# Performance work log

Measured on AMD Instinct MI355X. Metric: run time of the kernel, lower is better.

Reference implementation:

```python
import jax, jax.numpy as jnp
import numpy as np

D_MODEL = 768
N_HEADS = 12
D_K = D_MODEL // N_HEADS


def setup_inputs() -> dict:
    key = jax.random.key(0)
    ks = jax.random.split(key, 9)
    s = 1.0 / np.sqrt(D_MODEL)
    return {
        "x": jax.random.normal(ks[0], (2, 2048, D_MODEL), dtype=jnp.float32),
        "w_q": jax.random.normal(ks[1], (D_MODEL, D_MODEL), dtype=jnp.float32) * s,
        "b_q": jax.random.normal(ks[2], (D_MODEL,), dtype=jnp.float32) * 0.02,
        "w_k": jax.random.normal(ks[3], (D_MODEL, D_MODEL), dtype=jnp.float32) * s,
        "b_k": jax.random.normal(ks[4], (D_MODEL,), dtype=jnp.float32) * 0.02,
        "w_v": jax.random.normal(ks[5], (D_MODEL, D_MODEL), dtype=jnp.float32) * s,
        "b_v": jax.random.normal(ks[6], (D_MODEL,), dtype=jnp.float32) * 0.02,
        "w_o": jax.random.normal(ks[7], (D_MODEL, D_MODEL), dtype=jnp.float32) * s,
        "b_o": jax.random.normal(ks[8], (D_MODEL,), dtype=jnp.float32) * 0.02,
    }


def reference(x, w_q, b_q, w_k, b_k, w_v, b_v, w_o, b_o):
    B, S, _ = x.shape
    # nn.Linear: y = x @ W^T + b
    def proj(w, b):
        y = jnp.einsum("bsd,ed->bse", x, w) + b
        # [B, S, D] -> [B, H, S, d_k]
        return y.reshape(B, S, N_HEADS, D_K).transpose(0, 2, 1, 3)

    q = proj(w_q, b_q)
    k = proj(w_k, b_k)
    v = proj(w_v, b_v)

    scale = 1.0 / np.sqrt(D_K).astype(np.float32)
    scores = jnp.einsum("bhqd,bhkd->bhqk", q, k) * scale  # [B,H,S,S]
    attn = jax.nn.softmax(scores, axis=-1)
    ctx = jnp.einsum("bhqk,bhkd->bhqd", attn, v)  # [B,H,S,d_k]
    ctx = ctx.transpose(0, 2, 1, 3).reshape(B, S, D_MODEL)
    out = jnp.einsum("bsd,ed->bse", ctx, w_o) + b_o
    return out
```

## Files before the change

### kernel.cpp

```cpp
#include <hip/hip_runtime.h>
#include <hip/hip_bf16.h>

#define B_   2
#define S_   2048
#define D_   768
#define H_   12
#define DK_  64
#define R_   (B_*S_)
#define LOG2E_OVER8 0.18033688011112042f

typedef __attribute__((ext_vector_type(8))) short short8;
typedef __attribute__((ext_vector_type(4))) float f32x4;

__device__ __forceinline__ short f2b(float f) {
  union { float f; unsigned u; } x; x.f = f;
  unsigned r = x.u + 0x7fffu + ((x.u >> 16) & 1u);
  return (short)(r >> 16);
}

__device__ __forceinline__ unsigned cvt_pk_bf16(float lo, float hi) {
  unsigned r;
  asm("v_cvt_pk_bf16_f32 %0, %1, %2" : "=v"(r) : "v"(lo), "v"(hi));
  return r;
}

__device__ __forceinline__ void gl_lds16(const short* g, short* l) {
  __builtin_amdgcn_global_load_lds(
      (const __attribute__((address_space(1))) void*)g,
      (__attribute__((address_space(3))) void*)l, 16, 0, 0);
}

__global__ void cvt_kernel(const float* __restrict__ x,
                           const float* __restrict__ wq, const float* __restrict__ wk,
                           const float* __restrict__ wv, const float* __restrict__ wo,
                           short* __restrict__ xb, short* __restrict__ wb) {
  const int XQ = R_ * D_ / 4;
  const int WQ = D_ * D_ / 4;
  int idx = blockIdx.x * blockDim.x + threadIdx.x;
  const float* src; short* dst; int off;
  if (idx < XQ) { src = x; dst = xb; off = idx; }
  else {
    int wi = idx - XQ; int w = wi / WQ; off = wi - w * WQ;
    if      (w == 0) { src = wq; dst = wb; }
    else if (w == 1) { src = wk; dst = wb + D_*D_; }
    else if (w == 2) { src = wv; dst = wb + 2*D_*D_; }
    else             { src = wo; dst = wb + 3*D_*D_; }
  }
  float4 v = ((const float4*)src)[off];
  short4 o;
  o.x = f2b(v.x); o.y = f2b(v.y); o.z = f2b(v.z); o.w = f2b(v.w);
  ((short4*)dst)[off] = o;
}

__launch_bounds__(256)
__global__ void qkv_gemm_kernel(const short* __restrict__ xb, const short* __restrict__ wb,
                                const float* __restrict__ bq, const float* __restrict__ bk,
                                const float* __restrict__ bv,
                                short* __restrict__ Qw, short* __restrict__ Kw,
                                short* __restrict__ VTw) {
  __shared__ short As[2][128 * 32];
  __shared__ short Bs[2][128 * 32];
  const int which = blockIdx.z;
  const short* W = wb + which * (D_ * D_);
  const float* bias = (which == 0) ? bq : (which == 1) ? bk : bv;
  const int n0 = blockIdx.x * 128, m0 = blockIdx.y * 128;
  const int t = threadIdx.x, l = t & 63, w = t >> 6;
  const int wr = w >> 1, wc = w & 1;

  f32x4 acc[4][4] = {};
  const int srow = t >> 2, sseg = (t & 3) * 8;

#define GSTAGE(buf, k0) do { \
    gl_lds16(xb + (m0 + srow) * D_ + (k0) + sseg,      &As[buf][t * 8]); \
    gl_lds16(xb + (m0 + 64 + srow) * D_ + (k0) + sseg, &As[buf][(t + 256) * 8]); \
    gl_lds16(W  + (n0 + srow) * D_ + (k0) + sseg,      &Bs[buf][t * 8]); \
    gl_lds16(W  + (n0 + 64 + srow) * D_ + (k0) + sseg, &Bs[buf][(t + 256) * 8]); \
  } while (0)

  GSTAGE(0, 0);
  __syncthreads();
  int cur = 0;
  for (int k0 = 0; k0 < D_; k0 += 32) {
    if (k0 + 32 < D_) GSTAGE(cur ^ 1, k0 + 32);
    short8 a[4], b[4];
#pragma unroll
    for (int i = 0; i < 4; i++)
      a[i] = *(const short8*)&As[cur][(wr * 64 + i * 16 + (l & 15)) * 32 + (l >> 4) * 8];
#pragma unroll
    for (int i = 0; i < 4; i++)
      b[i] = *(const short8*)&Bs[cur][(wc * 64 + i * 16 + (l & 15)) * 32 + (l >> 4) * 8];
#pragma unroll
    for (int i = 0; i < 4; i++)
#pragma unroll
      for (int j = 0; j < 4; j++)
        acc[i][j] = __builtin_amdgcn_mfma_f32_16x16x32_bf16(a[i], b[j], acc[i][j], 0, 0, 0);
    __syncthreads();
    cur ^= 1;
  }
#undef GSTAGE

#pragma unroll
  for (int i = 0; i < 4; i++) {
#pragma unroll
    for (int j2 = 0; j2 < 4; j2++) {
      int mm = m0 + wr * 64 + i * 16 + (l >> 4) * 4 + j2;
      int bidx = mm >> 11, s = mm & 2047;
#pragma unroll
      for (int nj = 0; nj < 4; nj++) {
        int e = n0 + wc * 64 + nj * 16 + (l & 15);
        float val = acc[i][nj][j2] + bias[e];
        int h = e >> 6, dk = e & 63;
        int bh = bidx * H_ + h;
        if (which == 0)      Qw[(bh * S_ + s) * DK_ + dk] = f2b(val * LOG2E_OVER8);
        else if (which == 1) Kw[(bh * S_ + s) * DK_ + dk] = f2b(val);
        else                 VTw[(bh * DK_ + dk) * S_ + s] = f2b(val);
      }
    }
  }
}

#define KVB   32
#define SHALF 1024
__launch_bounds__(256, 3)
__global__ void attn_kernel(const short* __restrict__ Qw, const short* __restrict__ Kw,
                            const short* __restrict__ VTw, short* __restrict__ ctx) {
  __shared__ short Ksh[2][2][KVB * DK_];
  __shared__ short Vsh[2][2][KVB * DK_];

  const int t = threadIdx.x, l = t & 63, w = t >> 6;
  const int s = w >> 1, qh = w & 1;
  const int L = blockIdx.y * 32 + blockIdx.x;
  const int xcd = L & 7, idx = L >> 3;
  const int bh = xcd * 3 + (idx >> 5);
  const int qblk = idx & 31;
  const int q0 = qblk * 64 + qh * 32;
  const int bq = bh / H_, h = bh - bq * H_;
  const short* Qh = Qw + bh * S_ * DK_;
  const short* Kh = Kw + (bh * S_ + s * SHALF) * DK_;
  const short* Vh = VTw + bh * DK_ * S_ + s * SHALF;

  const int tt = t & 127;
  const int kr0 = tt >> 3, kc0 = tt & 7;
  const int koff0 = kr0 * DK_ + ((kc0 ^ (kr0 & 7)) << 3);
  const int vc8 = (tt & 7) ^ ((tt >> 3) & 7);
  const int vr0 = 2 * (tt >> 3) + (vc8 >> 2);
  const int voff0 = vr0 * S_ + ((vc8 & 3) << 3);

#define STAGE(buf, kt) do { \
    gl_lds16(Kh + (kt) * DK_ + koff0,        &Ksh[s][buf][tt * 8]); \
    gl_lds16(Kh + (kt) * DK_ + koff0 + 1024, &Ksh[s][buf][tt * 8 + 1024]); \
    gl_lds16(Vh + (kt) + voff0,              &Vsh[s][buf][tt * 8]); \
    gl_lds16(Vh + (kt) + voff0 + 32 * S_,    &Vsh[s][buf][tt * 8 + 1024]); \
  } while (0)

  short8 qf[2][2];
#pragma unroll
  for (int mi = 0; mi < 2; mi++)
#pragma unroll
    for (int ks = 0; ks < 2; ks++)
      qf[mi][ks] = *(const short8*)&Qh[(q0 + 16 * mi + (l & 15)) * DK_ + ks * 32 + (l >> 4) * 8];

  f32x4 acc_o[2][4] = {};
  float l_run[2] = {0.f, 0.f};

  STAGE(0, 0);
  __syncthreads();
  int cur = 0;

  for (int kt = 0; kt < SHALF; kt += KVB) {
    if (kt + KVB < SHALF) STAGE(cur ^ 1, kt + KVB);

    f32x4 acc_s[2][2] = {};
    __builtin_amdgcn_s_setprio(1);
#pragma unroll
    for (int ni = 0; ni < 2; ni++) {
      int r = (l & 15) + 16 * ni;
#pragma unroll
      for (int ks = 0; ks < 2; ks++) {
        int cc = (l >> 4) + 4 * ks;
        short8 kf = *(const short8*)&Ksh[s][cur][r * DK_ + ((cc ^ (r & 7)) << 3)];
        acc_s[0][ni] = __builtin_amdgcn_mfma_f32_16x16x32_bf16(kf, qf[0][ks], acc_s[0][ni], 0, 0, 0);
        acc_s[1][ni] = __builtin_amdgcn_mfma_f32_16x16x32_bf16(kf, qf[1][ks], acc_s[1][ni], 0, 0, 0);
      }
    }
    __builtin_amdgcn_s_setprio(0);

#pragma unroll
    for (int mi = 0; mi < 2; mi++) {
      float sum = 0.f;
#pragma unroll
      for (int ni = 0; ni < 2; ni++)
#pragma unroll
        for (int j = 0; j < 4; j++) {
          float p = __builtin_amdgcn_exp2f(acc_s[mi][ni][j]);
          acc_s[mi][ni][j] = p;
          sum += p;
        }
      l_run[mi] += sum;
    }

    union PK { unsigned u[4]; short8 v; } pa0, pa1;
    pa0.u[0] = cvt_pk_bf16(acc_s[0][0][0], acc_s[0][0][1]);
    pa0.u[1] = cvt_pk_bf16(acc_s[0][0][2], acc_s[0][0][3]);
    pa0.u[2] = cvt_pk_bf16(acc_s[0][1][0], acc_s[0][1][1]);
    pa0.u[3] = cvt_pk_bf16(acc_s[0][1][2], acc_s[0][1][3]);
    pa1.u[0] = cvt_pk_bf16(acc_s[1][0][0], acc_s[1][0][1]);
    pa1.u[1] = cvt_pk_bf16(acc_s[1][0][2], acc_s[1][0][3]);
    pa1.u[2] = cvt_pk_bf16(acc_s[1][1][0], acc_s[1][1][1]);
    pa1.u[3] = cvt_pk_bf16(acc_s[1][1][2], acc_s[1][1][3]);

    __builtin_amdgcn_s_setprio(1);
    {
      const int cc = l >> 4;
      union V8 { short4 h[2]; short8 v; };
#pragma unroll
      for (int nd = 0; nd < 4; nd++) {
        int vr = (l & 15) + 16 * nd, rp = vr >> 1;
        int ph0 = (((vr & 1) << 2) | (cc >> 1)) ^ (rp & 7);
        int ph1 = (((vr & 1) << 2) | (2 + (cc >> 1))) ^ (rp & 7);
        V8 vf;
        vf.h[0] = *(const short4*)&Vsh[s][cur][rp * 64 + ph0 * 8 + (cc & 1) * 4];
        vf.h[1] = *(const short4*)&Vsh[s][cur][rp * 64 + ph1 * 8 + (cc & 1) * 4];
        acc_o[0][nd] = __builtin_amdgcn_mfma_f32_16x16x32_bf16(pa0.v, vf.v, acc_o[0][nd], 0, 0, 0);
        acc_o[1][nd] = __builtin_amdgcn_mfma_f32_16x16x32_bf16(pa1.v, vf.v, acc_o[1][nd], 0, 0, 0);
      }
    }
    __builtin_amdgcn_s_setprio(0);

    __syncthreads();
    cur ^= 1;
  }

#pragma unroll
  for (int mi = 0; mi < 2; mi++) {
    l_run[mi] += __shfl_xor(l_run[mi], 16);
    l_run[mi] += __shfl_xor(l_run[mi], 32);
  }

  __syncthreads();
  float* Oshf = (float*)&Ksh[0][0][0];
  float* Lsh  = (float*)&Vsh[0][0][0];
  if (s == 1) {
#pragma unroll
    for (int mi = 0; mi < 2; mi++)
#pragma unroll
      for (int nd = 0; nd < 4; nd++)
#pragma unroll
        for (int j = 0; j < 4; j++)
          Oshf[qh * 2048 + (16 * mi + (l >> 4) * 4 + j) * 64 + (l & 15) + 16 * nd] = acc_o[mi][nd][j];
    if (l < 16) {
      Lsh[(qh * 2 + 0) * 16 + l] = l_run[0];
      Lsh[(qh * 2 + 1) * 16 + l] = l_run[1];
    }
  }
  __syncthreads();
  if (s == 0) {
#pragma unroll
    for (int mi = 0; mi < 2; mi++) {
#pragma unroll
      for (int j = 0; j < 4; j++) {
        int src = ((l >> 4) << 2) + j;
        float llo = __shfl(l_run[mi], src);
        float lhi = Lsh[(qh * 2 + mi) * 16 + src];
        float inv = 1.f / (llo + lhi);
        int srow = q0 + 16 * mi + src;
#pragma unroll
        for (int nd = 0; nd < 4; nd++) {
          float ohi = Oshf[qh * 2048 + (16 * mi + src) * 64 + (l & 15) + 16 * nd];
          float val = (acc_o[mi][nd][j] + ohi) * inv;
          ctx[(bq * S_ + srow) * D_ + h * DK_ + (l & 15) + 16 * nd] = f2b(val);
        }
      }
    }
  }
#undef STAGE
}

__launch_bounds__(256)
__global__ void oproj_kernel(const short* __restrict__ ctx, const short* __restrict__ Wo,
                             const float* __restrict__ bo, float* __restrict__ out) {
  __shared__ short As[2][128 * 32];
  __shared__ short Bs[2][128 * 32];
  const int n0 = blockIdx.x * 128, m0 = blockIdx.y * 128;
  const int t = threadIdx.x, l = t & 63, w = t >> 6;
  const int wr = w >> 1, wc = w & 1;

  f32x4 acc[4][4] = {};
  const int srow = t >> 2, sseg = (t & 3) * 8;

#define GSTAGE(buf, k0) do { \
    gl_lds16(ctx + (m0 + srow) * D_ + (k0) + sseg,      &As[buf][t * 8]); \
    gl_lds16(ctx + (m0 + 64 + srow) * D_ + (k0) + sseg, &As[buf][(t + 256) * 8]); \
    gl_lds16(Wo  + (n0 + srow) * D_ + (k0) + sseg,      &Bs[buf][t * 8]); \
    gl_lds16(Wo  + (n0 + 64 + srow) * D_ + (k0) + sseg, &Bs[buf][(t + 256) * 8]); \
  } while (0)

  GSTAGE(0, 0);
  __syncthreads();
  int cur = 0;
  for (int k0 = 0; k0 < D_; k0 += 32) {
    if (k0 + 32 < D_) GSTAGE(cur ^ 1, k0 + 32);
    short8 a[4], b[4];
#pragma unroll
    for (int i = 0; i < 4; i++)
      a[i] = *(const short8*)&As[cur][(wr * 64 + i * 16 + (l & 15)) * 32 + (l >> 4) * 8];
#pragma unroll
    for (int i = 0; i < 4; i++)
      b[i] = *(const short8*)&Bs[cur][(wc * 64 + i * 16 + (l & 15)) * 32 + (l >> 4) * 8];
#pragma unroll
    for (int i = 0; i < 4; i++)
#pragma unroll
      for (int j = 0; j < 4; j++)
        acc[i][j] = __builtin_amdgcn_mfma_f32_16x16x32_bf16(a[i], b[j], acc[i][j], 0, 0, 0);
    __syncthreads();
    cur ^= 1;
  }
#undef GSTAGE

#pragma unroll
  for (int i = 0; i < 4; i++) {
#pragma unroll
    for (int j2 = 0; j2 < 4; j2++) {
      int mm = m0 + wr * 64 + i * 16 + (l >> 4) * 4 + j2;
#pragma unroll
      for (int nj = 0; nj < 4; nj++) {
        int e = n0 + wc * 64 + nj * 16 + (l & 15);
        out[mm * D_ + e] = acc[i][nj][j2] + bo[e];
      }
    }
  }
}

extern "C" void kernel_launch(void* const* d_in, const int* in_sizes, int n_in,
                              void* d_out, int out_size, void* d_ws, size_t ws_size,
                              hipStream_t stream) {
  (void)in_sizes; (void)n_in; (void)out_size; (void)ws_size;
  const float* x  = (const float*)d_in[0];
  const float* wq = (const float*)d_in[1];
  const float* bq = (const float*)d_in[2];
  const float* wk = (const float*)d_in[3];
  const float* bk = (const float*)d_in[4];
  const float* wv = (const float*)d_in[5];
  const float* bv = (const float*)d_in[6];
  const float* wo = (const float*)d_in[7];
  const float* bo = (const float*)d_in[8];
  float* out = (float*)d_out;

  short* xb  = (short*)d_ws;
  short* wb  = xb + R_ * D_;
  short* Qw  = wb + 4 * D_ * D_;
  short* Kw  = Qw + R_ * D_;
  short* VTw = Kw + R_ * D_;
  short* ctx = VTw + R_ * D_;

  cvt_kernel<<<5376, 256, 0, stream>>>(x, wq, wk, wv, wo, xb, wb);
  qkv_gemm_kernel<<<dim3(6, 32, 3), 256, 0, stream>>>(xb, wb, bq, bk, bv, Qw, Kw, VTw);
  attn_kernel<<<dim3(32, 24), 256, 0, stream>>>(Qw, Kw, VTw, ctx);
  oproj_kernel<<<dim3(6, 32), 256, 0, stream>>>(ctx, wb + 3 * D_ * D_, bo, out);
}
```

Measured before the change: 97.40 us.

## Split attention KV range four ways per block, each wave covering all 64 queries

Restructures the attention kernel so each of the four waves takes a quarter of the key/value sequence (512 keys) and processes all 64 query rows, instead of two KV halves times two 32-row query halves. Each K/V fragment loaded from LDS now feeds four MFMAs instead of two, which cuts LDS read traffic per unit of compute. The cost is more accumulator registers per wave, occupancy lowered from 3 to 2 blocks, and a larger four-way partial sum reduction through shared memory at the end.

```diff
diff --git a/kernel.cpp b/kernel.cpp
--- a/kernel.cpp
+++ b/kernel.cpp
@@ -119,58 +119,58 @@
   }
 }
 
-#define KVB   32
-#define SHALF 1024
-__launch_bounds__(256, 3)
+#define KVB  32
+#define SQTR 512
+__launch_bounds__(256, 2)
 __global__ void attn_kernel(const short* __restrict__ Qw, const short* __restrict__ Kw,
                             const short* __restrict__ VTw, short* __restrict__ ctx) {
-  __shared__ short Ksh[2][2][KVB * DK_];
-  __shared__ short Vsh[2][2][KVB * DK_];
-
-  const int t = threadIdx.x, l = t & 63, w = t >> 6;
-  const int s = w >> 1, qh = w & 1;
+  __shared__ short Ksh[4][2][KVB * DK_];
+  __shared__ short Vsh[4][2][KVB * DK_];
+  __shared__ float Lsh[3][64];
+
+  const int t = threadIdx.x, l = t & 63, s = t >> 6;
   const int L = blockIdx.y * 32 + blockIdx.x;
   const int xcd = L & 7, idx = L >> 3;
   const int bh = xcd * 3 + (idx >> 5);
   const int qblk = idx & 31;
-  const int q0 = qblk * 64 + qh * 32;
+  const int q0 = qblk * 64;
   const int bq = bh / H_, h = bh - bq * H_;
   const short* Qh = Qw + bh * S_ * DK_;
-  const short* Kh = Kw + (bh * S_ + s * SHALF) * DK_;
-  const short* Vh = VTw + bh * DK_ * S_ + s * SHALF;
-
-  const int tt = t & 127;
-  const int kr0 = tt >> 3, kc0 = tt & 7;
-  const int koff0 = kr0 * DK_ + ((kc0 ^ (kr0 & 7)) << 3);
-  const int vc8 = (tt & 7) ^ ((tt >> 3) & 7);
-  const int vr0 = 2 * (tt >> 3) + (vc8 >> 2);
+  const short* Kh = Kw + (bh * S_ + s * SQTR) * DK_;
+  const short* Vh = VTw + bh * DK_ * S_ + s * SQTR;
+
+  const int c0 = l & 7, r0 = l >> 3;
+  const int koff0 = r0 * DK_ + ((c0 ^ r0) << 3);
+  const int vc8 = c0 ^ r0;
+  const int vr0 = 2 * r0 + (vc8 >> 2);
   const int voff0 = vr0 * S_ + ((vc8 & 3) << 3);
 
 #define STAGE(buf, kt) do { \
-    gl_lds16(Kh + (kt) * DK_ + koff0,        &Ksh[s][buf][tt * 8]); \
-    gl_lds16(Kh + (kt) * DK_ + koff0 + 1024, &Ksh[s][buf][tt * 8 + 1024]); \
-    gl_lds16(Vh + (kt) + voff0,              &Vsh[s][buf][tt * 8]); \
-    gl_lds16(Vh + (kt) + voff0 + 32 * S_,    &Vsh[s][buf][tt * 8 + 1024]); \
+    _Pragma("unroll") \
+    for (int j = 0; j < 4; j++) { \
+      gl_lds16(Kh + (kt) * DK_ + koff0 + 512 * j, &Ksh[s][buf][l * 8 + 512 * j]); \
+      gl_lds16(Vh + (kt) + voff0 + 16 * S_ * j,   &Vsh[s][buf][l * 8 + 512 * j]); \
+    } \
   } while (0)
 
-  short8 qf[2][2];
-#pragma unroll
-  for (int mi = 0; mi < 2; mi++)
+  short8 qf[4][2];
+#pragma unroll
+  for (int mi = 0; mi < 4; mi++)
 #pragma unroll
     for (int ks = 0; ks < 2; ks++)
       qf[mi][ks] = *(const short8*)&Qh[(q0 + 16 * mi + (l & 15)) * DK_ + ks * 32 + (l >> 4) * 8];
 
-  f32x4 acc_o[2][4] = {};
-  float l_run[2] = {0.f, 0.f};
+  f32x4 acc_o[4][4] = {};
+  float l_run[4] = {0.f, 0.f, 0.f, 0.f};
 
   STAGE(0, 0);
   __syncthreads();
   int cur = 0;
 
-  for (int kt = 0; kt < SHALF; kt += KVB) {
-    if (kt + KVB < SHALF) STAGE(cur ^ 1, kt + KVB);
-
-    f32x4 acc_s[2][2] = {};
+  for (int kt = 0; kt < SQTR; kt += KVB) {
+    if (kt + KVB < SQTR) STAGE(cur ^ 1, kt + KVB);
+
+    f32x4 acc_s[4][2] = {};
     __builtin_amdgcn_s_setprio(1);
 #pragma unroll
     for (int ni = 0; ni < 2; ni++) {
@@ -179,14 +179,16 @@
       for (int ks = 0; ks < 2; ks++) {
         int cc = (l >> 4) + 4 * ks;
         short8 kf = *(const short8*)&Ksh[s][cur][r * DK_ + ((cc ^ (r & 7)) << 3)];
-        acc_s[0][ni] = __builtin_amdgcn_mfma_f32_16x16x32_bf16(kf, qf[0][ks], acc_s[0][ni], 0, 0, 0);
-        acc_s[1][ni] = __builtin_amdgcn_mfma_f32_16x16x32_bf16(kf, qf[1][ks], acc_s[1][ni], 0, 0, 0);
+#pragma unroll
+        for (int mi = 0; mi < 4; mi++)
+          acc_s[mi][ni] = __builtin_amdgcn_mfma_f32_16x16x32_bf16(kf, qf[mi][ks], acc_s[mi][ni], 0, 0, 0);
       }
     }
     __builtin_amdgcn_s_setprio(0);
 
-#pragma unroll
-    for (int mi = 0; mi < 2; mi++) {
+    union PK { unsigned u[4]; short8 v; } pa[4];
+#pragma unroll
+    for (int mi = 0; mi < 4; mi++) {
       float sum = 0.f;
 #pragma unroll
       for (int ni = 0; ni < 2; ni++)
@@ -197,17 +199,11 @@
           sum += p;
         }
       l_run[mi] += sum;
-    }
-
-    union PK { unsigned u[4]; short8 v; } pa0, pa1;
-    pa0.u[0] = cvt_pk_bf16(acc_s[0][0][0], acc_s[0][0][1]);
-    pa0.u[1] = cvt_pk_bf16(acc_s[0][0][2], acc_s[0][0][3]);
-    pa0.u[2] = cvt_pk_bf16(acc_s[0][1][0], acc_s[0][1][1]);
-    pa0.u[3] = cvt_pk_bf16(acc_s[0][1][2], acc_s[0][1][3]);
-    pa1.u[0] = cvt_pk_bf16(acc_s[1][0][0], acc_s[1][0][1]);
-    pa1.u[1] = cvt_pk_bf16(acc_s[1][0][2], acc_s[1][0][3]);
-    pa1.u[2] = cvt_pk_bf16(acc_s[1][1][0], acc_s[1][1][1]);
-    pa1.u[3] = cvt_pk_bf16(acc_s[1][1][2], acc_s[1][1][3]);
+      pa[mi].u[0] = cvt_pk_bf16(acc_s[mi][0][0], acc_s[mi][0][1]);
+      pa[mi].u[1] = cvt_pk_bf16(acc_s[mi][0][2], acc_s[mi][0][3]);
+      pa[mi].u[2] = cvt_pk_bf16(acc_s[mi][1][0], acc_s[mi][1][1]);
+      pa[mi].u[3] = cvt_pk_bf16(acc_s[mi][1][2], acc_s[mi][1][3]);
+    }
 
     __builtin_amdgcn_s_setprio(1);
     {
@@ -221,8 +217,9 @@
         V8 vf;
         vf.h[0] = *(const short4*)&Vsh[s][cur][rp * 64 + ph0 * 8 + (cc & 1) * 4];
         vf.h[1] = *(const short4*)&Vsh[s][cur][rp * 64 + ph1 * 8 + (cc & 1) * 4];
-        acc_o[0][nd] = __builtin_amdgcn_mfma_f32_16x16x32_bf16(pa0.v, vf.v, acc_o[0][nd], 0, 0, 0);
-        acc_o[1][nd] = __builtin_amdgcn_mfma_f32_16x16x32_bf16(pa1.v, vf.v, acc_o[1][nd], 0, 0, 0);
+#pragma unroll
+        for (int mi = 0; mi < 4; mi++)
+          acc_o[mi][nd] = __builtin_amdgcn_mfma_f32_16x16x32_bf16(pa[mi].v, vf.v, acc_o[mi][nd], 0, 0, 0);
       }
     }
     __builtin_amdgcn_s_setprio(0);
@@ -232,43 +229,44 @@
   }
 
 #pragma unroll
-  for (int mi = 0; mi < 2; mi++) {
+  for (int mi = 0; mi < 4; mi++) {
     l_run[mi] += __shfl_xor(l_run[mi], 16);
     l_run[mi] += __shfl_xor(l_run[mi], 32);
   }
 
   __syncthreads();
-  float* Oshf = (float*)&Ksh[0][0][0];
-  float* Lsh  = (float*)&Vsh[0][0][0];
-  if (s == 1) {
-#pragma unroll
-    for (int mi = 0; mi < 2; mi++)
+  float* O12 = (float*)&Ksh[0][0][0];
+  float* O3  = (float*)&Vsh[0][0][0];
+  if (s >= 1) {
+    float* dst = (s == 1) ? O12 : (s == 2) ? O12 + 4096 : O3;
+#pragma unroll
+    for (int mi = 0; mi < 4; mi++)
 #pragma unroll
       for (int nd = 0; nd < 4; nd++)
 #pragma unroll
         for (int j = 0; j < 4; j++)
-          Oshf[qh * 2048 + (16 * mi + (l >> 4) * 4 + j) * 64 + (l & 15) + 16 * nd] = acc_o[mi][nd][j];
+          dst[(16 * mi + (l >> 4) * 4 + j) * 64 + (l & 15) + 16 * nd] = acc_o[mi][nd][j];
     if (l < 16) {
-      Lsh[(qh * 2 + 0) * 16 + l] = l_run[0];
-      Lsh[(qh * 2 + 1) * 16 + l] = l_run[1];
+#pragma unroll
+      for (int mi = 0; mi < 4; mi++) Lsh[s - 1][16 * mi + l] = l_run[mi];
     }
   }
   __syncthreads();
   if (s == 0) {
 #pragma unroll
-    for (int mi = 0; mi < 2; mi++) {
+    for (int mi = 0; mi < 4; mi++) {
 #pragma unroll
       for (int j = 0; j < 4; j++) {
         int src = ((l >> 4) << 2) + j;
-        float llo = __shfl(l_run[mi], src);
-        float lhi = Lsh[(qh * 2 + mi) * 16 + src];
-        float inv = 1.f / (llo + lhi);
-        int srow = q0 + 16 * mi + src;
+        int qrow = 16 * mi + src;
+        float lsum = __shfl(l_run[mi], src) + Lsh[0][qrow] + Lsh[1][qrow] + Lsh[2][qrow];
+        float inv = 1.f / lsum;
 #pragma unroll
         for (int nd = 0; nd < 4; nd++) {
-          float ohi = Oshf[qh * 2048 + (16 * mi + src) * 64 + (l & 15) + 16 * nd];
-          float val = (acc_o[mi][nd][j] + ohi) * inv;
-          ctx[(bq * S_ + srow) * D_ + h * DK_ + (l & 15) + 16 * nd] = f2b(val);
+          int dcol = (l & 15) + 16 * nd;
+          float v = acc_o[mi][nd][j] + O12[qrow * 64 + dcol]
+                  + O12[4096 + qrow * 64 + dcol] + O3[qrow * 64 + dcol];
+          ctx[(bq * S_ + q0 + qrow) * D_ + h * DK_ + dcol] = f2b(v * inv);
         }
       }
     }
```

New measurement: 113.2 us. +16.2%, slower.

## Triple-buffer QKV and output-projection GEMM staging with explicit vmcnt waits

Applied to the files above, without the earlier changes.

Moves the QKV projection and output projection GEMMs from double to triple LDS buffering. Two k-tiles are prefetched ahead, with a partial s_waitcnt vmcnt(4) and a single barrier per iteration, so global-to-LDS loads overlap with MFMA work across more stages. This removes the second __syncthreads per step and lets loads run further ahead. In exchange it uses 1.5x the LDS per block, which may lower occupancy, and correctness depends on hand-counted vmcnt values.

```diff
diff --git a/kernel.cpp b/kernel.cpp
--- a/kernel.cpp
+++ b/kernel.cpp
@@ -58,8 +58,8 @@
                                 const float* __restrict__ bv,
                                 short* __restrict__ Qw, short* __restrict__ Kw,
                                 short* __restrict__ VTw) {
-  __shared__ short As[2][128 * 32];
-  __shared__ short Bs[2][128 * 32];
+  __shared__ short As[3][128 * 32];
+  __shared__ short Bs[3][128 * 32];
   const int which = blockIdx.z;
   const short* W = wb + which * (D_ * D_);
   const float* bias = (which == 0) ? bq : (which == 1) ? bk : bv;
@@ -78,24 +78,33 @@
   } while (0)
 
   GSTAGE(0, 0);
-  __syncthreads();
-  int cur = 0;
-  for (int k0 = 0; k0 < D_; k0 += 32) {
-    if (k0 + 32 < D_) GSTAGE(cur ^ 1, k0 + 32);
+  GSTAGE(1, 32);
+  int step = 0;
+#pragma unroll 1
+  for (int k0 = 0; k0 < D_; k0 += 32, step++) {
+    if (k0 + 32 < D_) {
+      asm volatile("s_waitcnt vmcnt(4)" ::: "memory");
+    } else {
+      asm volatile("s_waitcnt vmcnt(0)" ::: "memory");
+    }
+    __builtin_amdgcn_sched_barrier(0);
+    __builtin_amdgcn_s_barrier();
+    if (k0 + 64 < D_) GSTAGE((step + 2) % 3, k0 + 64);
+    const int cb = step % 3;
     short8 a[4], b[4];
 #pragma unroll
     for (int i = 0; i < 4; i++)
-      a[i] = *(const short8*)&As[cur][(wr * 64 + i * 16 + (l & 15)) * 32 + (l >> 4) * 8];
-#pragma unroll
-    for (int i = 0; i < 4; i++)
-      b[i] = *(const short8*)&Bs[cur][(wc * 64 + i * 16 + (l & 15)) * 32 + (l >> 4) * 8];
+      a[i] = *(const short8*)&As[cb][(wr * 64 + i * 16 + (l & 15)) * 32 + (l >> 4) * 8];
+#pragma unroll
+    for (int i = 0; i < 4; i++)
+      b[i] = *(const short8*)&Bs[cb][(wc * 64 + i * 16 + (l & 15)) * 32 + (l >> 4) * 8];
 #pragma unroll
     for (int i = 0; i < 4; i++)
 #pragma unroll
       for (int j = 0; j < 4; j++)
         acc[i][j] = __builtin_amdgcn_mfma_f32_16x16x32_bf16(a[i], b[j], acc[i][j], 0, 0, 0);
-    __syncthreads();
-    cur ^= 1;
+    asm volatile("s_waitcnt lgkmcnt(0)" ::: "memory");
+    __builtin_amdgcn_sched_barrier(0);
   }
 #undef GSTAGE
 
@@ -279,8 +288,8 @@
 __launch_bounds__(256)
 __global__ void oproj_kernel(const short* __restrict__ ctx, const short* __restrict__ Wo,
                              const float* __restrict__ bo, float* __restrict__ out) {
-  __shared__ short As[2][128 * 32];
-  __shared__ short Bs[2][128 * 32];
+  __shared__ short As[3][128 * 32];
+  __shared__ short Bs[3][128 * 32];
   const int n0 = blockIdx.x * 128, m0 = blockIdx.y * 128;
   const int t = threadIdx.x, l = t & 63, w = t >> 6;
   const int wr = w >> 1, wc = w & 1;
@@ -296,24 +305,33 @@
   } while (0)
 
   GSTAGE(0, 0);
-  __syncthreads();
-  int cur = 0;
-  for (int k0 = 0; k0 < D_; k0 += 32) {
-    if (k0 + 32 < D_) GSTAGE(cur ^ 1, k0 + 32);
+  GSTAGE(1, 32);
+  int step = 0;
+#pragma unroll 1
+  for (int k0 = 0; k0 < D_; k0 += 32, step++) {
+    if (k0 + 32 < D_) {
+      asm volatile("s_waitcnt vmcnt(4)" ::: "memory");
+    } else {
+      asm volatile("s_waitcnt vmcnt(0)" ::: "memory");
+    }
+    __builtin_amdgcn_sched_barrier(0);
+    __builtin_amdgcn_s_barrier();
+    if (k0 + 64 < D_) GSTAGE((step + 2) % 3, k0 + 64);
+    const int cb = step % 3;
     short8 a[4], b[4];
 #pragma unroll
     for (int i = 0; i < 4; i++)
-      a[i] = *(const short8*)&As[cur][(wr * 64 + i * 16 + (l & 15)) * 32 + (l >> 4) * 8];
-#pragma unroll
-    for (int i = 0; i < 4; i++)
-      b[i] = *(const short8*)&Bs[cur][(wc * 64 + i * 16 + (l & 15)) * 32 + (l >> 4) * 8];
+      a[i] = *(const short8*)&As[cb][(wr * 64 + i * 16 + (l & 15)) * 32 + (l >> 4) * 8];
+#pragma unroll
+    for (int i = 0; i < 4; i++)
+      b[i] = *(const short8*)&Bs[cb][(wc * 64 + i * 16 + (l & 15)) * 32 + (l >> 4) * 8];
 #pragma unroll
     for (int i = 0; i < 4; i++)
 #pragma unroll
       for (int j = 0; j < 4; j++)
         acc[i][j] = __builtin_amdgcn_mfma_f32_16x16x32_bf16(a[i], b[j], acc[i][j], 0, 0, 0);
-    __syncthreads();
-    cur ^= 1;
+    asm volatile("s_waitcnt lgkmcnt(0)" ::: "memory");
+    __builtin_amdgcn_sched_barrier(0);
   }
 #undef GSTAGE
 
```

Result: slower. 101.0 us (+3.7%).

## Use BK=64 XOR-swizzled LDS tiles in projection GEMMs and smaller oproj tiles

Applied to the files above, without the earlier changes.

Both projection GEMMs now stage 64-wide K slices instead of 32, which halves the number of barrier-separated iterations. The LDS layout uses an XOR swizzle on 16-byte chunks to avoid bank conflicts on the MFMA fragment reads. The output projection switches to 64x128 tiles with each wave owning a 32-column strip, which doubles its grid from 192 to 384 blocks for better CU occupancy. LDS use per block doubles in the QKV kernel, which may reduce how many blocks fit on a CU.

```diff
diff --git a/kernel.cpp b/kernel.cpp
--- a/kernel.cpp
+++ b/kernel.cpp
@@ -58,8 +58,8 @@
                                 const float* __restrict__ bv,
                                 short* __restrict__ Qw, short* __restrict__ Kw,
                                 short* __restrict__ VTw) {
-  __shared__ short As[2][128 * 32];
-  __shared__ short Bs[2][128 * 32];
+  __shared__ short As[2][128 * 64];
+  __shared__ short Bs[2][128 * 64];
   const int which = blockIdx.z;
   const short* W = wb + which * (D_ * D_);
   const float* bias = (which == 0) ? bq : (which == 1) ? bk : bv;
@@ -68,32 +68,44 @@
   const int wr = w >> 1, wc = w & 1;
 
   f32x4 acc[4][4] = {};
-  const int srow = t >> 2, sseg = (t & 3) * 8;
+
+  const int sr0 = t >> 3, sc0 = t & 7;
+  const int soff = sr0 * D_ + ((sc0 ^ (sr0 & 7)) << 3);
 
 #define GSTAGE(buf, k0) do { \
-    gl_lds16(xb + (m0 + srow) * D_ + (k0) + sseg,      &As[buf][t * 8]); \
-    gl_lds16(xb + (m0 + 64 + srow) * D_ + (k0) + sseg, &As[buf][(t + 256) * 8]); \
-    gl_lds16(W  + (n0 + srow) * D_ + (k0) + sseg,      &Bs[buf][t * 8]); \
-    gl_lds16(W  + (n0 + 64 + srow) * D_ + (k0) + sseg, &Bs[buf][(t + 256) * 8]); \
+    _Pragma("unroll") \
+    for (int j = 0; j < 4; j++) { \
+      gl_lds16(xb + (m0 + 32 * j) * D_ + soff + (k0), &As[buf][(t + 256 * j) * 8]); \
+      gl_lds16(W  + (n0 + 32 * j) * D_ + soff + (k0), &Bs[buf][(t + 256 * j) * 8]); \
+    } \
   } while (0)
 
   GSTAGE(0, 0);
   __syncthreads();
   int cur = 0;
-  for (int k0 = 0; k0 < D_; k0 += 32) {
-    if (k0 + 32 < D_) GSTAGE(cur ^ 1, k0 + 32);
-    short8 a[4], b[4];
-#pragma unroll
-    for (int i = 0; i < 4; i++)
-      a[i] = *(const short8*)&As[cur][(wr * 64 + i * 16 + (l & 15)) * 32 + (l >> 4) * 8];
-#pragma unroll
-    for (int i = 0; i < 4; i++)
-      b[i] = *(const short8*)&Bs[cur][(wc * 64 + i * 16 + (l & 15)) * 32 + (l >> 4) * 8];
-#pragma unroll
-    for (int i = 0; i < 4; i++)
-#pragma unroll
-      for (int j = 0; j < 4; j++)
-        acc[i][j] = __builtin_amdgcn_mfma_f32_16x16x32_bf16(a[i], b[j], acc[i][j], 0, 0, 0);
+  for (int k0 = 0; k0 < D_; k0 += 64) {
+    if (k0 + 64 < D_) GSTAGE(cur ^ 1, k0 + 64);
+#pragma unroll
+    for (int kk = 0; kk < 2; kk++) {
+      short8 a[4], b[4];
+#pragma unroll
+      for (int i = 0; i < 4; i++) {
+        int R = wr * 64 + i * 16 + (l & 15);
+        int g = kk * 4 + (l >> 4);
+        a[i] = *(const short8*)&As[cur][R * 64 + ((g ^ (R & 7)) << 3)];
+      }
+#pragma unroll
+      for (int i = 0; i < 4; i++) {
+        int R = wc * 64 + i * 16 + (l & 15);
+        int g = kk * 4 + (l >> 4);
+        b[i] = *(const short8*)&Bs[cur][R * 64 + ((g ^ (R & 7)) << 3)];
+      }
+#pragma unroll
+      for (int i = 0; i < 4; i++)
+#pragma unroll
+        for (int j = 0; j < 4; j++)
+          acc[i][j] = __builtin_amdgcn_mfma_f32_16x16x32_bf16(a[i], b[j], acc[i][j], 0, 0, 0);
+    }
     __syncthreads();
     cur ^= 1;
   }
@@ -279,39 +291,51 @@
 __launch_bounds__(256)
 __global__ void oproj_kernel(const short* __restrict__ ctx, const short* __restrict__ Wo,
                              const float* __restrict__ bo, float* __restrict__ out) {
-  __shared__ short As[2][128 * 32];
-  __shared__ short Bs[2][128 * 32];
-  const int n0 = blockIdx.x * 128, m0 = blockIdx.y * 128;
+  __shared__ short As[2][64 * 64];
+  __shared__ short Bs[2][128 * 64];
+  const int n0 = blockIdx.x * 128, m0 = blockIdx.y * 64;
   const int t = threadIdx.x, l = t & 63, w = t >> 6;
-  const int wr = w >> 1, wc = w & 1;
-
-  f32x4 acc[4][4] = {};
-  const int srow = t >> 2, sseg = (t & 3) * 8;
+
+  f32x4 acc[4][2] = {};
+
+  const int sr0 = t >> 3, sc0 = t & 7;
+  const int soff = sr0 * D_ + ((sc0 ^ (sr0 & 7)) << 3);
 
 #define GSTAGE(buf, k0) do { \
-    gl_lds16(ctx + (m0 + srow) * D_ + (k0) + sseg,      &As[buf][t * 8]); \
-    gl_lds16(ctx + (m0 + 64 + srow) * D_ + (k0) + sseg, &As[buf][(t + 256) * 8]); \
-    gl_lds16(Wo  + (n0 + srow) * D_ + (k0) + sseg,      &Bs[buf][t * 8]); \
-    gl_lds16(Wo  + (n0 + 64 + srow) * D_ + (k0) + sseg, &Bs[buf][(t + 256) * 8]); \
+    _Pragma("unroll") \
+    for (int j = 0; j < 2; j++) \
+      gl_lds16(ctx + (m0 + 32 * j) * D_ + soff + (k0), &As[buf][(t + 256 * j) * 8]); \
+    _Pragma("unroll") \
+    for (int j = 0; j < 4; j++) \
+      gl_lds16(Wo + (n0 + 32 * j) * D_ + soff + (k0), &Bs[buf][(t + 256 * j) * 8]); \
   } while (0)
 
   GSTAGE(0, 0);
   __syncthreads();
   int cur = 0;
-  for (int k0 = 0; k0 < D_; k0 += 32) {
-    if (k0 + 32 < D_) GSTAGE(cur ^ 1, k0 + 32);
-    short8 a[4], b[4];
-#pragma unroll
-    for (int i = 0; i < 4; i++)
-      a[i] = *(const short8*)&As[cur][(wr * 64 + i * 16 + (l & 15)) * 32 + (l >> 4) * 8];
-#pragma unroll
-    for (int i = 0; i < 4; i++)
-      b[i] = *(const short8*)&Bs[cur][(wc * 64 + i * 16 + (l & 15)) * 32 + (l >> 4) * 8];
-#pragma unroll
-    for (int i = 0; i < 4; i++)
-#pragma unroll
-      for (int j = 0; j < 4; j++)
-        acc[i][j] = __builtin_amdgcn_mfma_f32_16x16x32_bf16(a[i], b[j], acc[i][j], 0, 0, 0);
+  for (int k0 = 0; k0 < D_; k0 += 64) {
+    if (k0 + 64 < D_) GSTAGE(cur ^ 1, k0 + 64);
+#pragma unroll
+    for (int kk = 0; kk < 2; kk++) {
+      short8 a[4], b[2];
+#pragma unroll
+      for (int i = 0; i < 4; i++) {
+        int R = i * 16 + (l & 15);
+        int g = kk * 4 + (l >> 4);
+        a[i] = *(const short8*)&As[cur][R * 64 + ((g ^ (R & 7)) << 3)];
+      }
+#pragma unroll
+      for (int nj = 0; nj < 2; nj++) {
+        int R = w * 32 + nj * 16 + (l & 15);
+        int g = kk * 4 + (l >> 4);
+        b[nj] = *(const short8*)&Bs[cur][R * 64 + ((g ^ (R & 7)) << 3)];
+      }
+#pragma unroll
+      for (int i = 0; i < 4; i++)
+#pragma unroll
+        for (int nj = 0; nj < 2; nj++)
+          acc[i][nj] = __builtin_amdgcn_mfma_f32_16x16x32_bf16(a[i], b[nj], acc[i][nj], 0, 0, 0);
+    }
     __syncthreads();
     cur ^= 1;
   }
@@ -321,10 +345,10 @@
   for (int i = 0; i < 4; i++) {
 #pragma unroll
     for (int j2 = 0; j2 < 4; j2++) {
-      int mm = m0 + wr * 64 + i * 16 + (l >> 4) * 4 + j2;
-#pragma unroll
-      for (int nj = 0; nj < 4; nj++) {
-        int e = n0 + wc * 64 + nj * 16 + (l & 15);
+      int mm = m0 + i * 16 + (l >> 4) * 4 + j2;
+#pragma unroll
+      for (int nj = 0; nj < 2; nj++) {
+        int e = n0 + w * 32 + nj * 16 + (l & 15);
         out[mm * D_ + e] = acc[i][nj][j2] + bo[e];
       }
     }
@@ -356,5 +380,5 @@
   cvt_kernel<<<5376, 256, 0, stream>>>(x, wq, wk, wv, wo, xb, wb);
   qkv_gemm_kernel<<<dim3(6, 32, 3), 256, 0, stream>>>(xb, wb, bq, bk, bv, Qw, Kw, VTw);
   attn_kernel<<<dim3(32, 24), 256, 0, stream>>>(Qw, Kw, VTw, ctx);
-  oproj_kernel<<<dim3(6, 32), 256, 0, stream>>>(ctx, wb + 3 * D_ * D_, bo, out);
-}
+  oproj_kernel<<<dim3(6, 64), 256, 0, stream>>>(ctx, wb + 3 * D_ * D_, bo, out);
+}
```

Measured after the change: 102.7 us. 5.4% more time.
